# Performance work log

Measured on AMD Instinct MI355X. Metric: run time of the kernel, lower is better.

## Reference

```python
import jax, jax.numpy as jnp
import numpy as np

TEMPERATURE = 1.0
EPS = 1e-8

def setup_inputs() -> dict:
    key = jax.random.key(0)
    k1, k2, k3 = jax.random.split(key, 3)
    B, A, D = 1024, 64, 1024
    q_embeddings = jax.random.normal(k1, (B, D), dtype=jnp.float32)
    a_list_embeddings = jax.random.normal(k2, (B, A, D), dtype=jnp.float32)
    a_list_scores = jax.random.uniform(k3, (B, A), dtype=jnp.float32)
    return {"q_embeddings": q_embeddings,
            "a_list_embeddings": a_list_embeddings,
            "a_list_scores": a_list_scores}

def _dcg(order, scores):
    # order: [B, A] indices (descending sort), scores: [B, A]
    A = scores.shape[-1]
    ranks = jnp.arange(1, A + 1, dtype=scores.dtype)  # [A]
    gain = jnp.take_along_axis(scores, order, axis=-1)  # [B, A]
    return jnp.sum(gain / jnp.log2(ranks + 1.0), axis=-1)  # [B]

def reference(q_embeddings, a_list_embeddings, a_list_scores):
    # sim[b, a] = q[b] . answers[b, a] / T
    sim = jnp.einsum('bd,bad->ba', q_embeddings, a_list_embeddings) / TEMPERATURE
    sim_probs = jax.nn.softmax(sim, axis=-1)                       # [B, A]
    target_probs = jax.nn.softmax(a_list_scores / TEMPERATURE, -1)  # [B, A]
    log_pred = jnp.log(sim_probs + EPS)
    # KL(target || pred) with reduction='sum' per sample
    kl = jnp.sum(target_probs * (jnp.log(target_probs) - log_pred), axis=-1)  # [B]
    loss = jnp.mean(kl)
    # NDCG metric
    pred_order = jnp.argsort(-sim, axis=-1)
    ideal_order = jnp.argsort(-a_list_scores, axis=-1)
    pred_dcg = _dcg(pred_order, a_list_scores)
    ideal_dcg = _dcg(ideal_order, a_list_scores)
    avg_ndcg = jnp.mean(pred_dcg / (ideal_dcg + EPS))
    return loss, avg_ndcg
```

## Files before the change

kernel.cpp:

```cpp
#include <hip/hip_runtime.h>
#include <math.h>

constexpr int B = 1024;
constexpr int A = 64;
constexpr int D = 1024;
constexpr float EPS = 1e-8f;

__device__ __forceinline__ float wave_reduce_sum(float v) {
    #pragma unroll
    for (int off = 32; off > 0; off >>= 1) v += __shfl_xor(v, off, 64);
    return v;
}
__device__ __forceinline__ float wave_reduce_max(float v) {
    #pragma unroll
    for (int off = 32; off > 0; off >>= 1) v = fmaxf(v, __shfl_xor(v, off, 64));
    return v;
}

__global__ __launch_bounds__(256, 6) void sim_kernel(
    const float* __restrict__ q,
    const float* __restrict__ emb,
    float* __restrict__ sims)
{
    const int b    = blockIdx.x >> 1;
    const int h    = blockIdx.x & 1;
    const int tid  = threadIdx.x;
    const int wave = tid >> 6;
    const int lane = tid & 63;

    const float4* q4 = reinterpret_cast<const float4*>(q + (size_t)b * D);
    const float4 qv0 = q4[lane];
    const float4 qv1 = q4[lane + 64];
    const float4 qv2 = q4[lane + 128];
    const float4 qv3 = q4[lane + 192];

    const int a0 = h * 32 + wave * 8;
    #pragma unroll 2
    for (int ai = 0; ai < 8; ++ai) {
        const int a = a0 + ai;
        const float4* e4 = reinterpret_cast<const float4*>(
            emb + ((size_t)b * A + a) * D);
        const float4 e0 = e4[lane];
        const float4 e1 = e4[lane + 64];
        const float4 e2 = e4[lane + 128];
        const float4 e3 = e4[lane + 192];
        float s0 = qv0.x*e0.x + qv0.y*e0.y + qv0.z*e0.z + qv0.w*e0.w;
        float s1 = qv1.x*e1.x + qv1.y*e1.y + qv1.z*e1.z + qv1.w*e1.w;
        float s2 = qv2.x*e2.x + qv2.y*e2.y + qv2.z*e2.z + qv2.w*e2.w;
        float s3 = qv3.x*e3.x + qv3.y*e3.y + qv3.z*e3.z + qv3.w*e3.w;
        float acc = (s0 + s1) + (s2 + s3);
        acc = wave_reduce_sum(acc);
        if (lane == 0) sims[(size_t)b * A + a] = acc;
    }
}

__global__ __launch_bounds__(256) void loss_kernel(
    const float* __restrict__ sims,
    const float* __restrict__ scores,
    float* __restrict__ kl_out,
    float* __restrict__ nd_out)
{
    const int tid  = threadIdx.x;
    const int wave = tid >> 6;
    const int lane = tid & 63;
    const int r    = blockIdx.x * 4 + wave;

    const int a = lane;
    const float s  = sims[(size_t)r * A + a];
    const float sc = scores[(size_t)r * A + a];

    const float m  = wave_reduce_max(s);
    const float ex = expf(s - m);
    const float se = wave_reduce_sum(ex);
    const float p  = ex / se;
    const float logp = logf(p + EPS);

    const float tm = wave_reduce_max(sc);
    const float te = expf(sc - tm);
    const float ts = wave_reduce_sum(te);
    const float t  = te / ts;
    const float logt = logf(t);

    const float kl = wave_reduce_sum(t * (logt - logp));

    int rp = 1, ri = 1;
    #pragma unroll
    for (int o = 0; o < 64; ++o) {
        const float so = __shfl(s,  o, 64);
        const float co = __shfl(sc, o, 64);
        rp += (so > s)  || (so == s  && o < a);
        ri += (co > sc) || (co == sc && o < a);
    }

    const float pd = wave_reduce_sum(sc / log2f((float)(rp + 1)));
    const float id = wave_reduce_sum(sc / log2f((float)(ri + 1)));

    if (lane == 0) {
        kl_out[r] = kl;
        nd_out[r] = pd / (id + EPS);
    }
}

__global__ __launch_bounds__(256) void final_kernel(
    const float* __restrict__ kl_in, const float* __restrict__ nd_in,
    float* __restrict__ out)
{
    const int tid  = threadIdx.x;
    const int wave = tid >> 6;
    const int lane = tid & 63;
    __shared__ float sk[4], sn[4];

    float kl = 0.f, nd = 0.f;
    for (int i = tid; i < B; i += 256) {
        kl += kl_in[i];
        nd += nd_in[i];
    }
    kl = wave_reduce_sum(kl);
    nd = wave_reduce_sum(nd);
    if (lane == 0) { sk[wave] = kl; sn[wave] = nd; }
    __syncthreads();
    if (tid == 0) {
        out[0] = (sk[0] + sk[1] + sk[2] + sk[3]) * (1.0f / B);
        out[1] = (sn[0] + sn[1] + sn[2] + sn[3]) * (1.0f / B);
    }
}

extern "C" void kernel_launch(void* const* d_in, const int* in_sizes, int n_in,
                              void* d_out, int out_size, void* d_ws, size_t ws_size,
                              hipStream_t stream) {
    const float* q      = (const float*)d_in[0];
    const float* emb    = (const float*)d_in[1];
    const float* scores = (const float*)d_in[2];
    float* out = (float*)d_out;

    float* sims = (float*)d_ws;
    float* kl_b = sims + (size_t)B * A;
    float* nd_b = kl_b + B;

    sim_kernel  <<<2 * B, 256, 0, stream>>>(q, emb, sims);
    loss_kernel <<<B / 4, 256, 0, stream>>>(sims, scores, kl_b, nd_b);
    final_kernel<<<1,     256, 0, stream>>>(kl_b, nd_b, out);
}
```

Baseline: 368.7 us.

## Fuse similarity and per-row loss/NDCG kernels into one block-per-row kernel

Merges the dot-product kernel and the softmax/KL/ranking kernel into a single kernel where each block handles one row, keeping similarities in shared memory instead of a global workspace. This removes one kernel launch and the global round-trip of the similarity matrix. In exchange the grid is halved (1024 blocks of 16 answers per wave), occupancy hint drops from 6 to 4, and only one wave does the tail loss work while the other three exit.

```diff
diff --git a/kernel.cpp b/kernel.cpp
--- a/kernel.cpp
+++ b/kernel.cpp
@@ -17,16 +17,19 @@
     return v;
 }
 
-__global__ __launch_bounds__(256, 6) void sim_kernel(
+__global__ __launch_bounds__(256, 4) void rank_fused(
     const float* __restrict__ q,
     const float* __restrict__ emb,
-    float* __restrict__ sims)
+    const float* __restrict__ scores,
+    float* __restrict__ kl_out,
+    float* __restrict__ nd_out)
 {
-    const int b    = blockIdx.x >> 1;
-    const int h    = blockIdx.x & 1;
+    const int b    = blockIdx.x;
     const int tid  = threadIdx.x;
     const int wave = tid >> 6;
     const int lane = tid & 63;
+
+    __shared__ float sim_s[A];
 
     const float4* q4 = reinterpret_cast<const float4*>(q + (size_t)b * D);
     const float4 qv0 = q4[lane];
@@ -34,9 +37,9 @@
     const float4 qv2 = q4[lane + 128];
     const float4 qv3 = q4[lane + 192];
 
-    const int a0 = h * 32 + wave * 8;
+    const int a0 = wave * 16;
     #pragma unroll 2
-    for (int ai = 0; ai < 8; ++ai) {
+    for (int ai = 0; ai < 16; ++ai) {
         const int a = a0 + ai;
         const float4* e4 = reinterpret_cast<const float4*>(
             emb + ((size_t)b * A + a) * D);
@@ -50,24 +53,15 @@
         float s3 = qv3.x*e3.x + qv3.y*e3.y + qv3.z*e3.z + qv3.w*e3.w;
         float acc = (s0 + s1) + (s2 + s3);
         acc = wave_reduce_sum(acc);
-        if (lane == 0) sims[(size_t)b * A + a] = acc;
+        if (lane == 0) sim_s[a] = acc;
     }
-}
+    __syncthreads();
 
-__global__ __launch_bounds__(256) void loss_kernel(
-    const float* __restrict__ sims,
-    const float* __restrict__ scores,
-    float* __restrict__ kl_out,
-    float* __restrict__ nd_out)
-{
-    const int tid  = threadIdx.x;
-    const int wave = tid >> 6;
-    const int lane = tid & 63;
-    const int r    = blockIdx.x * 4 + wave;
+    if (tid >= 64) return;
 
     const int a = lane;
-    const float s  = sims[(size_t)r * A + a];
-    const float sc = scores[(size_t)r * A + a];
+    const float s  = sim_s[a];
+    const float sc = scores[(size_t)b * A + a];
 
     const float m  = wave_reduce_max(s);
     const float ex = expf(s - m);
@@ -96,8 +90,8 @@
     const float id = wave_reduce_sum(sc / log2f((float)(ri + 1)));
 
     if (lane == 0) {
-        kl_out[r] = kl;
-        nd_out[r] = pd / (id + EPS);
+        kl_out[b] = kl;
+        nd_out[b] = pd / (id + EPS);
     }
 }
 
@@ -133,11 +127,9 @@
     const float* scores = (const float*)d_in[2];
     float* out = (float*)d_out;
 
-    float* sims = (float*)d_ws;
-    float* kl_b = sims + (size_t)B * A;
+    float* kl_b = (float*)d_ws;
     float* nd_b = kl_b + B;
 
-    sim_kernel  <<<2 * B, 256, 0, stream>>>(q, emb, sims);
-    loss_kernel <<<B / 4, 256, 0, stream>>>(sims, scores, kl_b, nd_b);
-    final_kernel<<<1,     256, 0, stream>>>(kl_b, nd_b, out);
+    rank_fused  <<<B, 256, 0, stream>>>(q, emb, scores, kl_b, nd_b);
+    final_kernel<<<1, 256, 0, stream>>>(kl_b, nd_b, out);
 }
```

New measurement: 371.0 us. No clear change (+0.6%).
